# Kernel optimization log

Measured on AMD Instinct MI355X. Metric: run time of the kernel, lower is better.

Reference implementation:

```python
import jax, jax.numpy as jnp
import numpy as np

T = 4096          # tokens (batch*seq)
DIM = 2048        # model dim
INTER = 1024      # moe_inter_dim
E = 32            # n_routed_experts
TOPK = 6          # n_activated_experts
G = 8             # n_expert_groups
TOPK_G = 4        # n_limited_groups
SHARED_INTER = 2 * INTER  # n_shared_experts * moe_inter_dim
ROUTE_SCALE = 1.0


def setup_inputs() -> dict:
    key = jax.random.key(0)
    ks = jax.random.split(key, 8)
    s = 0.02
    return {
        "x": jax.random.normal(ks[0], (T, DIM), jnp.float32),
        "gate_w": jax.random.normal(ks[1], (E, DIM), jnp.float32) * s,
        "wg": jax.random.normal(ks[2], (E, DIM, INTER), jnp.float32) * s,   # gate_proj (stored [in,out])
        "wu": jax.random.normal(ks[3], (E, DIM, INTER), jnp.float32) * s,   # up_proj
        "wd": jax.random.normal(ks[4], (E, INTER, DIM), jnp.float32) * s,   # down_proj
        "swg": jax.random.normal(ks[5], (DIM, SHARED_INTER), jnp.float32) * s,
        "swu": jax.random.normal(ks[6], (DIM, SHARED_INTER), jnp.float32) * s,
        "swd": jax.random.normal(ks[7], (SHARED_INTER, DIM), jnp.float32) * s,
    }


def _gate(x, gate_w):
    # scores = softmax(x @ W^T); bias is None since dim != 7168 -> group score = amax
    scores = jax.nn.softmax(x @ gate_w.T, axis=-1)          # [T, E]
    orig = scores
    gs = scores.reshape(x.shape[0], G, E // G)              # [T, G, E/G]
    group_scores = gs.max(axis=-1)                          # [T, G]
    _, gidx = jax.lax.top_k(group_scores, TOPK_G)           # [T, TOPK_G]
    gmask = jnp.zeros((x.shape[0], G), bool).at[
        jnp.arange(x.shape[0])[:, None], gidx].set(True)
    masked = jnp.where(gmask[:, :, None], gs, -jnp.inf).reshape(x.shape[0], E)
    _, idx = jax.lax.top_k(masked, TOPK)                    # [T, TOPK]
    w = jnp.take_along_axis(orig, idx, axis=1) * ROUTE_SCALE  # softmax path: no renorm
    return w, idx


def reference(x, gate_w, wg, wu, wd, swg, swu, swd):
    weights, indices = _gate(x, gate_w)
    # combine[t, e] = routing weight of expert e for token t (0 if not selected)
    combine = (jax.nn.one_hot(indices, E, dtype=x.dtype) * weights[..., None]).sum(axis=1)  # [T, E]
    y = jnp.zeros_like(x)
    for e in range(E):  # fixed small loop over structurally distinct expert params
        h = jax.nn.silu(x @ wg[e]) * (x @ wu[e])            # [T, INTER]
        y = y + (h @ wd[e]) * combine[:, e:e + 1]
    shared = (jax.nn.silu(x @ swg) * (x @ swu)) @ swd       # shared experts MLP
    return y + shared
```

## Files before the change

kernel.cpp:

```cpp
#include <hip/hip_runtime.h>
#include <hip/hip_bf16.h>

typedef float f32x4 __attribute__((ext_vector_type(4)));
typedef __bf16 bf16x8 __attribute__((ext_vector_type(8)));
typedef unsigned short u16;

#define T_TOK 4096
#define DIMK 2048
#define INTERN 1024
#define NEXP 32
#define NTOPK 6
#define NGRP 8
#define NTOPG 4
#define SINTER 2048
#define MAXPADROWS 29184

__device__ __forceinline__ void glds16(const void* g, void* l) {
    auto* gp = (const __attribute__((address_space(1))) int*)(g);
    auto* lp = (__attribute__((address_space(3))) int*)(l);
    __builtin_amdgcn_global_load_lds(gp, lp, 16, 0, 0);
}

__device__ __forceinline__ size_t toff(int row, int k, int K) {
    int g = (k >> 3) & 7;
// ... 109 lines not shown
    float mx = sc[0];
#pragma unroll
    for (int e = 1; e < NEXP; ++e) mx = fmaxf(mx, sc[e]);
    float ssum = 0.f;
#pragma unroll
    for (int e = 0; e < NEXP; ++e) { sc[e] = __expf(sc[e] - mx); ssum += sc[e]; }
    const float inv = 1.f / ssum;
    float gsc[NGRP];
#pragma unroll
    for (int g = 0; g < NGRP; ++g) {
        float m2 = sc[g * 4];
#pragma unroll
        for (int j = 1; j < 4; ++j) m2 = fmaxf(m2, sc[g * 4 + j]);
        gsc[g] = m2;
    }
    int gsel = 0;
    for (int r = 0; r < NTOPG; ++r) {
        float bv = -1.f; int bi = 0;
#pragma unroll
        for (int g = 0; g < NGRP; ++g) {
            bool c = (((gsel >> g) & 1) == 0) && (gsc[g] > bv);
            bv = c ? gsc[g] : bv; bi = c ? g : bi;
        }
        gsel |= (1 << bi);
    }
    float msk[NEXP];
#pragma unroll
    for (int e = 0; e < NEXP; ++e) msk[e] = ((gsel >> (e >> 2)) & 1) ? sc[e] : -1.f;
    for (int r = 0; r < NTOPK; ++r) {
        float bv = -3.f; int bi = 0;
#pragma unroll
        for (int e = 0; e < NEXP; ++e) {
            bool c = msk[e] > bv;
            bv = c ? msk[e] : bv; bi = c ? e : bi;
        }
#pragma unroll
        for (int e = 0; e < NEXP; ++e) if (e == bi) msk[e] = -2.f;
        float w = bv * inv;
        int slot = atomicAdd(&counts[bi], 1);
        ids[bi * T_TOK + slot] = t;
        tok2row[t * NTOPK + r] = (bi << 12) | slot;
        wtok[t * NTOPK + r] = w;
    }
}

__global__ void scan_kernel(const int* __restrict__ counts, int* __restrict__ poff) {
    if (threadIdx.x == 0) {
        int o = 0;
        for (int e = 0; e < NEXP; ++e) { poff[e] = o; o += (counts[e] + 127) & ~127; }
    }
}


__global__ __launch_bounds__(1024, 1) void gemm1_fused_kernel(
    const u16* __restrict__ xbT, const u16* __restrict__ WcatE, u16* __restrict__ H,
    const u16* __restrict__ WcatS, u16* __restrict__ Hs,
    const int* __restrict__ counts, const int* __restrict__ poff, const int* __restrict__ ids) {
    __shared__ u16 Alds[2 * 16384];
    __shared__ u16 Blds[2 * 16384];
    constexpr int NT = DIMK / 64;

    int bm, bn, M, Mpad, hbase, HKdim, e = 0;
    const u16* b0;
    u16* ho;
    bool gath;
    if (blockIdx.z < 32) {
        int lin = blockIdx.x + 16 * (blockIdx.y + 8 * blockIdx.z);
        e = 31 - (((lin >> 10) << 3) | (lin & 7));
        int j = (lin >> 3) & 127;
        bm = j & 15; bn = j >> 4;
        M = counts[e];
        if (bm * 256 >= M) return;
        Mpad = (M + 127) & ~127;
        hbase = poff[e];
        b0 = WcatE + (size_t)e * 2048 * DIMK;
        ho = H; HKdim = INTERN; gath = true;
    } else {
        int lin = blockIdx.x + 16 * (blockIdx.y + 8 * (blockIdx.z - 32));
        int swz = (lin & 7) * 32 + (lin >> 3);
        bm = swz & 15; bn = swz >> 4;
        M = T_TOK; Mpad = T_TOK; hbase = 0;
        b0 = WcatS; ho = Hs; HKdim = SINTER; gath = false;
    }

    const int tid = threadIdx.x;
    const int srow = tid >> 3, sp = tid & 7;
    size_t aSrc[2];
#pragma unroll
    for (int h = 0; h < 2; ++h) {
        int row = bm * 256 + h * 128 + srow;
        int tok;
        if (gath) { int cr = row < M ? row : M - 1; tok = ids[e * T_TOK + cr]; }
        else tok = row;
        int gsw = sp ^ (srow & 7) ^ (tok & 7);
        aSrc[h] = (size_t)(tok >> 7) * (128 * 2048) + (size_t)((tok & 127) * 64 + (gsw << 3));
    }
    const u16* bCh[2] = { b0 + (size_t)(2 * bn + 0) * (128 * 2048), b0 + (size_t)(2 * bn + 1) * (128 * 2048) };
    const int t8 = tid * 8;

    const int lane = tid & 63, wv = tid >> 6;
    const int wr = wv >> 2, wc = wv & 3;
    const int l15 = lane & 15, lk = lane >> 4;

    f32x4 acc[4][4];
#pragma unroll
    for (int m = 0; m < 4; ++m)
#pragma unroll
        for (int n = 0; n < 4; ++n) acc[m][n] = {0.f, 0.f, 0.f, 0.f};

    auto STGALL = [&](int kt, int buf) {
        glds16(xbT + aSrc[0] + (size_t)kt * 8192, &Alds[buf * 16384 + t8]);
        glds16(xbT + aSrc[1] + (size_t)kt * 8192, &Alds[buf * 16384 + 8192 + t8]);
        glds16(bCh[0] + (size_t)kt * 8192 + t8, &Blds[buf * 16384 + t8]);
        glds16(bCh[1] + (size_t)kt * 8192 + t8, &Blds[buf * 16384 + 8192 + t8]);
    };
    bf16x8 afr[4][2], bfr[2][2];
    auto DSRA = [&](int buf) {
#pragma unroll
        for (int mi = 0; mi < 4; ++mi)
#pragma unroll
            for (int ki = 0; ki < 2; ++ki) {
                int rl = wr * 64 + mi * 16 + l15;
                int g = ki * 4 + lk;
                afr[mi][ki] = *reinterpret_cast<const bf16x8*>(
                    &Alds[buf * 16384 + (rl >> 7) * 8192 + (rl & 127) * 64 + ((g ^ (rl & 7)) << 3)]);
            }
    };
    auto DSRB = [&](int buf, int nh) {
#pragma unroll
        for (int nj = 0; nj < 2; ++nj)
#pragma unroll
            for (int ki = 0; ki < 2; ++ki) {
                int rc = wc * 64 + (nh * 2 + nj) * 16 + l15;
                int g = ki * 4 + lk;
                bfr[nj][ki] = *reinterpret_cast<const bf16x8*>(
                    &Blds[buf * 16384 + (rc >> 7) * 8192 + (rc & 127) * 64 + ((g ^ (rc & 7)) << 3)]);
            }
    };

    STGALL(0, 0);
    STGALL(1, 1);

#pragma unroll 1
    for (int i = 0; i < NT; ++i) {
        const int buf = i & 1;
        if (i + 1 < NT) {
            asm volatile("s_waitcnt vmcnt(4)" ::: "memory");
        } else {
            asm volatile("s_waitcnt vmcnt(0)" ::: "memory");
        }
        __builtin_amdgcn_s_barrier();
        __builtin_amdgcn_sched_barrier(0);
        DSRA(buf);
        DSRB(buf, 0);
        __builtin_amdgcn_s_setprio(1);
#pragma unroll
        for (int ki = 0; ki < 2; ++ki)
#pragma unroll
            for (int mi = 0; mi < 4; ++mi)
#pragma unroll
                for (int nj = 0; nj < 2; ++nj)
                    acc[mi][nj] = __builtin_amdgcn_mfma_f32_16x16x32_bf16(afr[mi][ki], bfr[nj][ki], acc[mi][nj], 0, 0, 0);
        __builtin_amdgcn_s_setprio(0);
        DSRB(buf, 1);
        __builtin_amdgcn_s_setprio(1);
#pragma unroll
        for (int ki = 0; ki < 2; ++ki)
#pragma unroll
            for (int mi = 0; mi < 4; ++mi)
#pragma unroll
                for (int nj = 0; nj < 2; ++nj)
                    acc[mi][2 + nj] = __builtin_amdgcn_mfma_f32_16x16x32_bf16(afr[mi][ki], bfr[nj][ki], acc[mi][2 + nj], 0, 0, 0);
        __builtin_amdgcn_s_setprio(0);
        __builtin_amdgcn_sched_barrier(0);
        __builtin_amdgcn_s_barrier();
        __builtin_amdgcn_sched_barrier(0);
        if (i + 2 < NT) STGALL(i + 2, buf);
    }

#pragma unroll
    for (int mi = 0; mi < 4; ++mi) {
#pragma unroll
        for (int r = 0; r < 4; ++r) {
            int grow = bm * 256 + wr * 64 + mi * 16 + lk * 4 + r;
            if (grow < Mpad) {
#pragma unroll
                for (int nh = 0; nh < 2; ++nh) {
                    float gg = acc[mi][nh * 2 + 0][r];
                    float uu = acc[mi][nh * 2 + 1][r];
                    float h = gg / (1.f + __expf(-gg)) * uu;
                    int n = bn * 256 + wc * 64 + nh * 32 + l15;
                    int jcol = ((n >> 5) << 4) + (n & 15);
                    __bf16 hb = (__bf16)h;
                    ho[toff(hbase + grow, jcol, HKdim)] = __builtin_bit_cast(u16, hb);
                }
            }
        }
    }
}

__global__ __launch_bounds__(1024, 1) void gemm2_fused_kernel(
    const u16* __restrict__ H, const u16* __restrict__ wdT, u16* __restrict__ Ye,
    const u16* __restrict__ Hs, const u16* __restrict__ swdT, u16* __restrict__ Yss,
    const int* __restrict__ counts, const int* __restrict__ poff) {
    __shared__ u16 Alds[2 * 16384];
    __shared__ u16 Blds[2 * 16384];
    constexpr int NT = 16;

    int bm, bn, M, rowbase, AKK, kt0;
    const u16 *aBase, *bBase;
    u16* yo;
    if (blockIdx.z < 32) {
        int lin = blockIdx.x + 16 * (blockIdx.y + 8 * blockIdx.z);
        int e = 31 - (((lin >> 10) << 3) | (lin & 7));
        int j = (lin >> 3) & 127;
        bm = j & 15; bn = j >> 4;
        M = counts[e];
        if (bm * 256 >= M) return;
        rowbase = poff[e];
        aBase = H + (size_t)poff[e] * INTERN;
        bBase = wdT + (size_t)e * 2048 * INTERN;
        yo = Ye; AKK = INTERN; kt0 = 0;
    } else {
        int lin = blockIdx.x + 16 * (blockIdx.y + 8 * (blockIdx.z - 32));
        int swz = (lin & 7) * 32 + (lin >> 3);
        bm = swz & 15; bn = (swz >> 4) & 7;
        int ks = swz >> 7;
        M = T_TOK; rowbase = ks * T_TOK;
        aBase = Hs; bBase = swdT; yo = Yss; AKK = SINTER; kt0 = ks * 16;
    }
    const u16* aCh[2] = { aBase + (size_t)(2 * bm + 0) * (size_t)(128 * AKK) + (size_t)kt0 * 8192,
                          aBase + (size_t)(2 * bm + 1) * (size_t)(128 * AKK) + (size_t)kt0 * 8192 };
    const u16* bCh[2] = { bBase + (size_t)(2 * bn + 0) * (size_t)(128 * AKK) + (size_t)kt0 * 8192,
                          bBase + (size_t)(2 * bn + 1) * (size_t)(128 * AKK) + (size_t)kt0 * 8192 };
    const int tid = threadIdx.x;
    const int t8 = tid * 8;
    const int lane = tid & 63, wv = tid >> 6;
    const int wr = wv >> 2, wc = wv & 3;
    const int l15 = lane & 15, lk = lane >> 4;

    f32x4 acc[4][4];
#pragma unroll
    for (int m = 0; m < 4; ++m)
#pragma unroll
        for (int n = 0; n < 4; ++n) acc[m][n] = {0.f, 0.f, 0.f, 0.f};

    auto STGALL = [&](int kt, int buf) {
        glds16(aCh[0] + (size_t)kt * 8192 + t8, &Alds[buf * 16384 + t8]);
        glds16(aCh[1] + (size_t)kt * 8192 + t8, &Alds[buf * 16384 + 8192 + t8]);
        glds16(bCh[0] + (size_t)kt * 8192 + t8, &Blds[buf * 16384 + t8]);
        glds16(bCh[1] + (size_t)kt * 8192 + t8, &Blds[buf * 16384 + 8192 + t8]);
    };
    bf16x8 afr[4][2], bfr[2][2];
    auto DSRA = [&](int buf) {
#pragma unroll
        for (int mi = 0; mi < 4; ++mi)
#pragma unroll
            for (int ki = 0; ki < 2; ++ki) {
                int rl = wr * 64 + mi * 16 + l15;
                int g = ki * 4 + lk;
                afr[mi][ki] = *reinterpret_cast<const bf16x8*>(
                    &Alds[buf * 16384 + (rl >> 7) * 8192 + (rl & 127) * 64 + ((g ^ (rl & 7)) << 3)]);
            }
    };
    auto DSRB = [&](int buf, int nh) {
#pragma unroll
        for (int nj = 0; nj < 2; ++nj)
#pragma unroll
            for (int ki = 0; ki < 2; ++ki) {
                int rc = wc * 64 + (nh * 2 + nj) * 16 + l15;
                int g = ki * 4 + lk;
                bfr[nj][ki] = *reinterpret_cast<const bf16x8*>(
                    &Blds[buf * 16384 + (rc >> 7) * 8192 + (rc & 127) * 64 + ((g ^ (rc & 7)) << 3)]);
            }
    };

    STGALL(0, 0);
    STGALL(1, 1);

#pragma unroll 1
    for (int i = 0; i < NT; ++i) {
        const int buf = i & 1;
        if (i + 1 < NT) {
            asm volatile("s_waitcnt vmcnt(4)" ::: "memory");
        } else {
            asm volatile("s_waitcnt vmcnt(0)" ::: "memory");
        }
        __builtin_amdgcn_s_barrier();
        __builtin_amdgcn_sched_barrier(0);
        DSRA(buf);
        DSRB(buf, 0);
        __builtin_amdgcn_s_setprio(1);
#pragma unroll
        for (int ki = 0; ki < 2; ++ki)
#pragma unroll
            for (int mi = 0; mi < 4; ++mi)
#pragma unroll
                for (int nj = 0; nj < 2; ++nj)
                    acc[mi][nj] = __builtin_amdgcn_mfma_f32_16x16x32_bf16(afr[mi][ki], bfr[nj][ki], acc[mi][nj], 0, 0, 0);
        __builtin_amdgcn_s_setprio(0);
        DSRB(buf, 1);
        __builtin_amdgcn_s_setprio(1);
#pragma unroll
        for (int ki = 0; ki < 2; ++ki)
#pragma unroll
            for (int mi = 0; mi < 4; ++mi)
#pragma unroll
                for (int nj = 0; nj < 2; ++nj)
                    acc[mi][2 + nj] = __builtin_amdgcn_mfma_f32_16x16x32_bf16(afr[mi][ki], bfr[nj][ki], acc[mi][2 + nj], 0, 0, 0);
        __builtin_amdgcn_s_setprio(0);
        __builtin_amdgcn_sched_barrier(0);
        __builtin_amdgcn_s_barrier();
        __builtin_amdgcn_sched_barrier(0);
        if (i + 2 < NT) STGALL(i + 2, buf);
    }

#pragma unroll
    for (int mi = 0; mi < 4; ++mi) {
#pragma unroll
        for (int r = 0; r < 4; ++r) {
            int grow = bm * 256 + wr * 64 + mi * 16 + lk * 4 + r;
            if (grow < M) {
                u16* yr = yo + (size_t)(rowbase + grow) * 2048;
#pragma unroll
                for (int ni = 0; ni < 4; ++ni) {
                    int col = bn * 256 + wc * 64 + ni * 16 + l15;
                    __bf16 yb = (__bf16)acc[mi][ni][r];
                    yr[col] = __builtin_bit_cast(u16, yb);
                }
            }
        }
    }
}

__global__ __launch_bounds__(256) void combine_kernel(const u16* __restrict__ Yss, const u16* __restrict__ Ye,
                                                      const int* __restrict__ tok2row, const float* __restrict__ wtok,
                                                      const int* __restrict__ poff, float* __restrict__ out) {
    const int t = blockIdx.x;
    const int c = threadIdx.x * 8;
    bf16x8 v0 = *reinterpret_cast<const bf16x8*>(Yss + (size_t)t * 2048 + c);
    bf16x8 v1 = *reinterpret_cast<const bf16x8*>(Yss + (size_t)(T_TOK + t) * 2048 + c);
    float acc[8];
#pragma unroll
    for (int j = 0; j < 8; ++j) acc[j] = (float)v0[j] + (float)v1[j];
#pragma unroll
    for (int r = 0; r < NTOPK; ++r) {
        int pk = tok2row[t * NTOPK + r];
        int e = pk >> 12, sl = pk & 4095;
        int row = poff[e] + sl;
        float w = wtok[t * NTOPK + r];
        bf16x8 v = *reinterpret_cast<const bf16x8*>(Ye + (size_t)row * 2048 + c);
#pragma unroll
        for (int j = 0; j < 8; ++j) acc[j] += w * (float)v[j];
    }
    float4 o0 = {acc[0], acc[1], acc[2], acc[3]};
    float4 o1 = {acc[4], acc[5], acc[6], acc[7]};
    float4* po = reinterpret_cast<float4*>(out + (size_t)t * 2048 + c);
    po[0] = o0; po[1] = o1;
}

extern "C" void kernel_launch(void* const* d_in, const int* in_sizes, int n_in,
                              void* d_out, int out_size, void* d_ws, size_t ws_size,
                              hipStream_t stream) {
    const float* x = (const float*)d_in[0];
    const float* gate_w = (const float*)d_in[1];
    const float* wg = (const float*)d_in[2];
    const float* wu = (const float*)d_in[3];
    const float* wd = (const float*)d_in[4];
    const float* swg = (const float*)d_in[5];
    const float* swu = (const float*)d_in[6];
    const float* swd = (const float*)d_in[7];
    float* out = (float*)d_out;

    char* ws = (char*)d_ws;
    size_t off = 0;
    auto alloc = [&](size_t bytes) {
        void* p = ws + off;
        off = (off + bytes + 255) & ~(size_t)255;
        return p;
    };
    u16* xbT = (u16*)alloc((size_t)T_TOK * DIMK * 2);
    u16* H = (u16*)alloc((size_t)MAXPADROWS * INTERN * 2);
    u16* Hs = (u16*)alloc((size_t)T_TOK * SINTER * 2);
    u16* Ye = (u16*)alloc((size_t)MAXPADROWS * 2048 * 2);
    u16* Yss = (u16*)alloc((size_t)2 * T_TOK * 2048 * 2);
    int* ids = (int*)alloc((size_t)NEXP * T_TOK * 4);
    int* tok2row = (int*)alloc((size_t)T_TOK * NTOPK * 4);
    float* wtok = (float*)alloc((size_t)T_TOK * NTOPK * 4);
    int* counts = (int*)alloc(NEXP * 4);
    int* poff = (int*)alloc(NEXP * 4);
    u16* WcatS = (u16*)alloc((size_t)(2 * SINTER) * DIMK * 2);
    u16* swdT = (u16*)alloc((size_t)DIMK * SINTER * 2);
    u16* WcatE = (u16*)alloc((size_t)NEXP * (2 * INTERN) * DIMK * 2);
    u16* wdT = WcatE;

    hipMemsetAsync(counts, 0, NEXP * 4, stream);
    cast_x_tiled_kernel<<<(T_TOK * DIMK) / (256 * 8), 256, 0, stream>>>(x, xbT);
    gate_kernel<<<T_TOK, 64, 0, stream>>>(x, gate_w, counts, ids, tok2row, wtok);
    scan_kernel<<<1, 64, 0, stream>>>(counts, poff);

    cat_trans_kernel<DIMK, SINTER><<<dim3(SINTER / 32, DIMK / 64, 1), 256, 0, stream>>>(swg, swu, WcatS);
    cat_trans_kernel<DIMK, INTERN><<<dim3(INTERN / 32, DIMK / 64, NEXP), 256, 0, stream>>>(wg, wu, WcatE);
    trans_tiled_kernel<SINTER, DIMK><<<dim3(DIMK / 64, SINTER / 64, 1), 256, 0, stream>>>(swd, swdT);

    gemm1_fused_kernel<<<dim3(16, 8, 34), 1024, 0, stream>>>(
        xbT, WcatE, H, WcatS, Hs, counts, poff, ids);

    trans_tiled_kernel<INTERN, DIMK><<<dim3(DIMK / 64, INTERN / 64, NEXP), 256, 0, stream>>>(wd, wdT);

    gemm2_fused_kernel<<<dim3(16, 8, 34), 1024, 0, stream>>>(
        H, wdT, Ye, Hs, swdT, Yss, counts, poff);

    combine_kernel<<<T_TOK, 256, 0, stream>>>(Yss, Ye, tok2row, wtok, poff, out);
}
```

Baseline: 1.137 ms.

## Use 8-wave blocks with 128x64 warp tiles and interleaved staged prefetch

Both grouped GEMMs go from 16 waves to 8 waves per block. Each wave now computes a 128x64 sub-tile with twice as many accumulators. The main loop is split into four MFMA phases, and the next k-tile's A and B halves are loaded between them, in a ping-pong style schedule that overlaps global-to-LDS copies with compute. Launch bounds now allow two blocks per CU to raise occupancy, at the cost of more registers per wave and extra barriers.

```diff
diff --git a/kernel.cpp b/kernel.cpp
--- a/kernel.cpp
+++ b/kernel.cpp
@@ -185,7 +185,7 @@
 }
 
 
-__global__ __launch_bounds__(1024, 1) void gemm1_fused_kernel(
+__global__ __launch_bounds__(512, 2) void gemm1_fused_kernel(
     const u16* __restrict__ xbT, const u16* __restrict__ WcatE, u16* __restrict__ H,
     const u16* __restrict__ WcatS, u16* __restrict__ Hs,
     const int* __restrict__ counts, const int* __restrict__ poff, const int* __restrict__ ids) {
@@ -217,110 +217,136 @@
     }
 
     const int tid = threadIdx.x;
-    const int srow = tid >> 3, sp = tid & 7;
-    size_t aSrc[2];
-#pragma unroll
-    for (int h = 0; h < 2; ++h) {
-        int row = bm * 256 + h * 128 + srow;
-        int tok;
-        if (gath) { int cr = row < M ? row : M - 1; tok = ids[e * T_TOK + cr]; }
-        else tok = row;
-        int gsw = sp ^ (srow & 7) ^ (tok & 7);
-        aSrc[h] = (size_t)(tok >> 7) * (128 * 2048) + (size_t)((tok & 127) * 64 + (gsw << 3));
-    }
+    const int t8 = tid * 8;
+    size_t aSrc[2][2];
+#pragma unroll
+    for (int h = 0; h < 2; ++h)
+#pragma unroll
+        for (int j = 0; j < 2; ++j) {
+            int drow = j * 64 + (tid >> 3);
+            int row = bm * 256 + h * 128 + drow;
+            int tok;
+            if (gath) { int cr = row < M ? row : M - 1; tok = ids[e * T_TOK + cr]; }
+            else tok = row;
+            int slot = (tid & 7) ^ (drow & 7) ^ (tok & 7);
+            aSrc[h][j] = (size_t)(tok >> 7) * (size_t)(128 * 2048) + (size_t)((tok & 127) * 64 + slot * 8);
+        }
     const u16* bCh[2] = { b0 + (size_t)(2 * bn + 0) * (128 * 2048), b0 + (size_t)(2 * bn + 1) * (128 * 2048) };
-    const int t8 = tid * 8;
 
     const int lane = tid & 63, wv = tid >> 6;
     const int wr = wv >> 2, wc = wv & 3;
     const int l15 = lane & 15, lk = lane >> 4;
 
-    f32x4 acc[4][4];
-#pragma unroll
-    for (int m = 0; m < 4; ++m)
+    f32x4 acc[8][4];
+#pragma unroll
+    for (int m = 0; m < 8; ++m)
 #pragma unroll
         for (int n = 0; n < 4; ++n) acc[m][n] = {0.f, 0.f, 0.f, 0.f};
 
-    auto STGALL = [&](int kt, int buf) {
-        glds16(xbT + aSrc[0] + (size_t)kt * 8192, &Alds[buf * 16384 + t8]);
-        glds16(xbT + aSrc[1] + (size_t)kt * 8192, &Alds[buf * 16384 + 8192 + t8]);
-        glds16(bCh[0] + (size_t)kt * 8192 + t8, &Blds[buf * 16384 + t8]);
-        glds16(bCh[1] + (size_t)kt * 8192 + t8, &Blds[buf * 16384 + 8192 + t8]);
-    };
-    bf16x8 afr[4][2], bfr[2][2];
-    auto DSRA = [&](int buf) {
+    auto SA = [&](int kt, int h, int buf) {
+        glds16(xbT + aSrc[h][0] + (size_t)kt * 8192, &Alds[buf * 16384 + h * 8192 + t8]);
+        glds16(xbT + aSrc[h][1] + (size_t)kt * 8192, &Alds[buf * 16384 + h * 8192 + 4096 + t8]);
+    };
+    auto SB = [&](int kt, int h, int buf) {
+        glds16(bCh[h] + (size_t)kt * 8192 + t8, &Blds[buf * 16384 + h * 8192 + t8]);
+        glds16(bCh[h] + (size_t)kt * 8192 + 4096 + t8, &Blds[buf * 16384 + h * 8192 + 4096 + t8]);
+    };
+    bf16x8 afr[4][2], bfr0[2][2], bfr1[2][2];
+    auto DSRA = [&](int buf, int mh) {
 #pragma unroll
         for (int mi = 0; mi < 4; ++mi)
 #pragma unroll
             for (int ki = 0; ki < 2; ++ki) {
-                int rl = wr * 64 + mi * 16 + l15;
+                int rl = wr * 128 + mh * 64 + mi * 16 + l15;
                 int g = ki * 4 + lk;
                 afr[mi][ki] = *reinterpret_cast<const bf16x8*>(
                     &Alds[buf * 16384 + (rl >> 7) * 8192 + (rl & 127) * 64 + ((g ^ (rl & 7)) << 3)]);
             }
     };
-    auto DSRB = [&](int buf, int nh) {
+    auto DSRB = [&](int buf, int nh, bf16x8 (&bf)[2][2]) {
 #pragma unroll
         for (int nj = 0; nj < 2; ++nj)
 #pragma unroll
             for (int ki = 0; ki < 2; ++ki) {
                 int rc = wc * 64 + (nh * 2 + nj) * 16 + l15;
                 int g = ki * 4 + lk;
-                bfr[nj][ki] = *reinterpret_cast<const bf16x8*>(
+                bf[nj][ki] = *reinterpret_cast<const bf16x8*>(
                     &Blds[buf * 16384 + (rc >> 7) * 8192 + (rc & 127) * 64 + ((g ^ (rc & 7)) << 3)]);
             }
     };
 
-    STGALL(0, 0);
-    STGALL(1, 1);
+    SA(0, 0, 0); SA(0, 1, 0); SB(0, 0, 0); SB(0, 1, 0); SA(1, 0, 1);
+    asm volatile("s_waitcnt vmcnt(2)" ::: "memory");
+    __builtin_amdgcn_s_barrier();
 
 #pragma unroll 1
-    for (int i = 0; i < NT; ++i) {
-        const int buf = i & 1;
-        if (i + 1 < NT) {
-            asm volatile("s_waitcnt vmcnt(4)" ::: "memory");
-        } else {
-            asm volatile("s_waitcnt vmcnt(0)" ::: "memory");
-        }
-        __builtin_amdgcn_s_barrier();
-        __builtin_amdgcn_sched_barrier(0);
-        DSRA(buf);
-        DSRB(buf, 0);
-        __builtin_amdgcn_s_setprio(1);
-#pragma unroll
-        for (int ki = 0; ki < 2; ++ki)
-#pragma unroll
-            for (int mi = 0; mi < 4; ++mi)
-#pragma unroll
-                for (int nj = 0; nj < 2; ++nj)
-                    acc[mi][nj] = __builtin_amdgcn_mfma_f32_16x16x32_bf16(afr[mi][ki], bfr[nj][ki], acc[mi][nj], 0, 0, 0);
-        __builtin_amdgcn_s_setprio(0);
-        DSRB(buf, 1);
-        __builtin_amdgcn_s_setprio(1);
-#pragma unroll
-        for (int ki = 0; ki < 2; ++ki)
-#pragma unroll
-            for (int mi = 0; mi < 4; ++mi)
-#pragma unroll
-                for (int nj = 0; nj < 2; ++nj)
-                    acc[mi][2 + nj] = __builtin_amdgcn_mfma_f32_16x16x32_bf16(afr[mi][ki], bfr[nj][ki], acc[mi][2 + nj], 0, 0, 0);
-        __builtin_amdgcn_s_setprio(0);
-        __builtin_amdgcn_sched_barrier(0);
-        __builtin_amdgcn_s_barrier();
-        __builtin_amdgcn_sched_barrier(0);
-        if (i + 2 < NT) STGALL(i + 2, buf);
-    }
-
-#pragma unroll
-    for (int mi = 0; mi < 4; ++mi) {
+    for (int t = 0; t < NT; ++t) {
+        const int buf = t & 1;
+        DSRA(buf, 0);
+        DSRB(buf, 0, bfr0);
+        if (t + 1 < NT) SA(t + 1, 1, buf ^ 1);
+        __builtin_amdgcn_s_barrier();
+        __builtin_amdgcn_s_setprio(1);
+#pragma unroll
+        for (int ki = 0; ki < 2; ++ki)
+#pragma unroll
+            for (int mi = 0; mi < 4; ++mi)
+#pragma unroll
+                for (int nj = 0; nj < 2; ++nj)
+                    acc[mi][nj] = __builtin_amdgcn_mfma_f32_16x16x32_bf16(afr[mi][ki], bfr0[nj][ki], acc[mi][nj], 0, 0, 0);
+        __builtin_amdgcn_s_setprio(0);
+        __builtin_amdgcn_s_barrier();
+        DSRB(buf, 1, bfr1);
+        if (t + 1 < NT) SB(t + 1, 0, buf ^ 1);
+        __builtin_amdgcn_s_barrier();
+        __builtin_amdgcn_s_setprio(1);
+#pragma unroll
+        for (int ki = 0; ki < 2; ++ki)
+#pragma unroll
+            for (int mi = 0; mi < 4; ++mi)
+#pragma unroll
+                for (int nj = 0; nj < 2; ++nj)
+                    acc[mi][2 + nj] = __builtin_amdgcn_mfma_f32_16x16x32_bf16(afr[mi][ki], bfr1[nj][ki], acc[mi][2 + nj], 0, 0, 0);
+        __builtin_amdgcn_s_setprio(0);
+        __builtin_amdgcn_s_barrier();
+        DSRA(buf, 1);
+        if (t + 1 < NT) SB(t + 1, 1, buf ^ 1);
+        __builtin_amdgcn_s_barrier();
+        __builtin_amdgcn_s_setprio(1);
+#pragma unroll
+        for (int ki = 0; ki < 2; ++ki)
+#pragma unroll
+            for (int mi = 0; mi < 4; ++mi)
+#pragma unroll
+                for (int nj = 0; nj < 2; ++nj)
+                    acc[4 + mi][2 + nj] = __builtin_amdgcn_mfma_f32_16x16x32_bf16(afr[mi][ki], bfr1[nj][ki], acc[4 + mi][2 + nj], 0, 0, 0);
+        __builtin_amdgcn_s_setprio(0);
+        __builtin_amdgcn_s_barrier();
+        if (t + 2 < NT) SA(t + 2, 0, buf);
+        __builtin_amdgcn_s_setprio(1);
+#pragma unroll
+        for (int ki = 0; ki < 2; ++ki)
+#pragma unroll
+            for (int mi = 0; mi < 4; ++mi)
+#pragma unroll
+                for (int nj = 0; nj < 2; ++nj)
+                    acc[4 + mi][nj] = __builtin_amdgcn_mfma_f32_16x16x32_bf16(afr[mi][ki], bfr0[nj][ki], acc[4 + mi][nj], 0, 0, 0);
+        __builtin_amdgcn_s_setprio(0);
+        if (t + 2 < NT) { asm volatile("s_waitcnt vmcnt(2)" ::: "memory"); }
+        else { asm volatile("s_waitcnt vmcnt(0)" ::: "memory"); }
+        __builtin_amdgcn_s_barrier();
+    }
+
+#pragma unroll
+    for (int mI = 0; mI < 8; ++mI) {
 #pragma unroll
         for (int r = 0; r < 4; ++r) {
-            int grow = bm * 256 + wr * 64 + mi * 16 + lk * 4 + r;
+            int grow = bm * 256 + wr * 128 + mI * 16 + lk * 4 + r;
             if (grow < Mpad) {
 #pragma unroll
                 for (int nh = 0; nh < 2; ++nh) {
-                    float gg = acc[mi][nh * 2 + 0][r];
-                    float uu = acc[mi][nh * 2 + 1][r];
+                    float gg = acc[mI][nh * 2 + 0][r];
+                    float uu = acc[mI][nh * 2 + 1][r];
                     float h = gg / (1.f + __expf(-gg)) * uu;
                     int n = bn * 256 + wc * 64 + nh * 32 + l15;
                     int jcol = ((n >> 5) << 4) + (n & 15);
@@ -332,7 +358,7 @@
     }
 }
 
-__global__ __launch_bounds__(1024, 1) void gemm2_fused_kernel(
+__global__ __launch_bounds__(512, 2) void gemm2_fused_kernel(
     const u16* __restrict__ H, const u16* __restrict__ wdT, u16* __restrict__ Ye,
     const u16* __restrict__ Hs, const u16* __restrict__ swdT, u16* __restrict__ Yss,
     const int* __restrict__ counts, const int* __restrict__ poff) {
@@ -372,93 +398,117 @@
     const int wr = wv >> 2, wc = wv & 3;
     const int l15 = lane & 15, lk = lane >> 4;
 
-    f32x4 acc[4][4];
-#pragma unroll
-    for (int m = 0; m < 4; ++m)
+    f32x4 acc[8][4];
+#pragma unroll
+    for (int m = 0; m < 8; ++m)
 #pragma unroll
         for (int n = 0; n < 4; ++n) acc[m][n] = {0.f, 0.f, 0.f, 0.f};
 
-    auto STGALL = [&](int kt, int buf) {
-        glds16(aCh[0] + (size_t)kt * 8192 + t8, &Alds[buf * 16384 + t8]);
-        glds16(aCh[1] + (size_t)kt * 8192 + t8, &Alds[buf * 16384 + 8192 + t8]);
-        glds16(bCh[0] + (size_t)kt * 8192 + t8, &Blds[buf * 16384 + t8]);
-        glds16(bCh[1] + (size_t)kt * 8192 + t8, &Blds[buf * 16384 + 8192 + t8]);
-    };
-    bf16x8 afr[4][2], bfr[2][2];
-    auto DSRA = [&](int buf) {
+    auto SA = [&](int kt, int h, int buf) {
+        glds16(aCh[h] + (size_t)kt * 8192 + t8, &Alds[buf * 16384 + h * 8192 + t8]);
+        glds16(aCh[h] + (size_t)kt * 8192 + 4096 + t8, &Alds[buf * 16384 + h * 8192 + 4096 + t8]);
+    };
+    auto SB = [&](int kt, int h, int buf) {
+        glds16(bCh[h] + (size_t)kt * 8192 + t8, &Blds[buf * 16384 + h * 8192 + t8]);
+        glds16(bCh[h] + (size_t)kt * 8192 + 4096 + t8, &Blds[buf * 16384 + h * 8192 + 4096 + t8]);
+    };
+    bf16x8 afr[4][2], bfr0[2][2], bfr1[2][2];
+    auto DSRA = [&](int buf, int mh) {
 #pragma unroll
         for (int mi = 0; mi < 4; ++mi)
 #pragma unroll
             for (int ki = 0; ki < 2; ++ki) {
-                int rl = wr * 64 + mi * 16 + l15;
+                int rl = wr * 128 + mh * 64 + mi * 16 + l15;
                 int g = ki * 4 + lk;
                 afr[mi][ki] = *reinterpret_cast<const bf16x8*>(
                     &Alds[buf * 16384 + (rl >> 7) * 8192 + (rl & 127) * 64 + ((g ^ (rl & 7)) << 3)]);
             }
     };
-    auto DSRB = [&](int buf, int nh) {
+    auto DSRB = [&](int buf, int nh, bf16x8 (&bf)[2][2]) {
 #pragma unroll
         for (int nj = 0; nj < 2; ++nj)
 #pragma unroll
             for (int ki = 0; ki < 2; ++ki) {
                 int rc = wc * 64 + (nh * 2 + nj) * 16 + l15;
                 int g = ki * 4 + lk;
-                bfr[nj][ki] = *reinterpret_cast<const bf16x8*>(
+                bf[nj][ki] = *reinterpret_cast<const bf16x8*>(
                     &Blds[buf * 16384 + (rc >> 7) * 8192 + (rc & 127) * 64 + ((g ^ (rc & 7)) << 3)]);
             }
     };
 
-    STGALL(0, 0);
-    STGALL(1, 1);
+    SA(0, 0, 0); SA(0, 1, 0); SB(0, 0, 0); SB(0, 1, 0); SA(1, 0, 1);
+    asm volatile("s_waitcnt vmcnt(2)" ::: "memory");
+    __builtin_amdgcn_s_barrier();
 
 #pragma unroll 1
-    for (int i = 0; i < NT; ++i) {
-        const int buf = i & 1;
-        if (i + 1 < NT) {
-            asm volatile("s_waitcnt vmcnt(4)" ::: "memory");
-        } else {
-            asm volatile("s_waitcnt vmcnt(0)" ::: "memory");
-        }
-        __builtin_amdgcn_s_barrier();
-        __builtin_amdgcn_sched_barrier(0);
-        DSRA(buf);
-        DSRB(buf, 0);
-        __builtin_amdgcn_s_setprio(1);
-#pragma unroll
-        for (int ki = 0; ki < 2; ++ki)
-#pragma unroll
-            for (int mi = 0; mi < 4; ++mi)
-#pragma unroll
-                for (int nj = 0; nj < 2; ++nj)
-                    acc[mi][nj] = __builtin_amdgcn_mfma_f32_16x16x32_bf16(afr[mi][ki], bfr[nj][ki], acc[mi][nj], 0, 0, 0);
-        __builtin_amdgcn_s_setprio(0);
-        DSRB(buf, 1);
-        __builtin_amdgcn_s_setprio(1);
-#pragma unroll
-        for (int ki = 0; ki < 2; ++ki)
-#pragma unroll
-            for (int mi = 0; mi < 4; ++mi)
-#pragma unroll
-                for (int nj = 0; nj < 2; ++nj)
-                    acc[mi][2 + nj] = __builtin_amdgcn_mfma_f32_16x16x32_bf16(afr[mi][ki], bfr[nj][ki], acc[mi][2 + nj], 0, 0, 0);
-        __builtin_amdgcn_s_setprio(0);
-        __builtin_amdgcn_sched_barrier(0);
-        __builtin_amdgcn_s_barrier();
-        __builtin_amdgcn_sched_barrier(0);
-        if (i + 2 < NT) STGALL(i + 2, buf);
-    }
-
-#pragma unroll
-    for (int mi = 0; mi < 4; ++mi) {
+    for (int t = 0; t < NT; ++t) {
+        const int buf = t & 1;
+        DSRA(buf, 0);
+        DSRB(buf, 0, bfr0);
+        if (t + 1 < NT) SA(t + 1, 1, buf ^ 1);
+        __builtin_amdgcn_s_barrier();
+        __builtin_amdgcn_s_setprio(1);
+#pragma unroll
+        for (int ki = 0; ki < 2; ++ki)
+#pragma unroll
+            for (int mi = 0; mi < 4; ++mi)
+#pragma unroll
+                for (int nj = 0; nj < 2; ++nj)
+                    acc[mi][nj] = __builtin_amdgcn_mfma_f32_16x16x32_bf16(afr[mi][ki], bfr0[nj][ki], acc[mi][nj], 0, 0, 0);
+        __builtin_amdgcn_s_setprio(0);
+        __builtin_amdgcn_s_barrier();
+        DSRB(buf, 1, bfr1);
+        if (t + 1 < NT) SB(t + 1, 0, buf ^ 1);
+        __builtin_amdgcn_s_barrier();
+        __builtin_amdgcn_s_setprio(1);
+#pragma unroll
+        for (int ki = 0; ki < 2; ++ki)
+#pragma unroll
+            for (int mi = 0; mi < 4; ++mi)
+#pragma unroll
+                for (int nj = 0; nj < 2; ++nj)
+                    acc[mi][2 + nj] = __builtin_amdgcn_mfma_f32_16x16x32_bf16(afr[mi][ki], bfr1[nj][ki], acc[mi][2 + nj], 0, 0, 0);
+        __builtin_amdgcn_s_setprio(0);
+        __builtin_amdgcn_s_barrier();
+        DSRA(buf, 1);
+        if (t + 1 < NT) SB(t + 1, 1, buf ^ 1);
+        __builtin_amdgcn_s_barrier();
+        __builtin_amdgcn_s_setprio(1);
+#pragma unroll
+        for (int ki = 0; ki < 2; ++ki)
+#pragma unroll
+            for (int mi = 0; mi < 4; ++mi)
+#pragma unroll
+                for (int nj = 0; nj < 2; ++nj)
+                    acc[4 + mi][2 + nj] = __builtin_amdgcn_mfma_f32_16x16x32_bf16(afr[mi][ki], bfr1[nj][ki], acc[4 + mi][2 + nj], 0, 0, 0);
+        __builtin_amdgcn_s_setprio(0);
+        __builtin_amdgcn_s_barrier();
+        if (t + 2 < NT) SA(t + 2, 0, buf);
+        __builtin_amdgcn_s_setprio(1);
+#pragma unroll
+        for (int ki = 0; ki < 2; ++ki)
+#pragma unroll
+            for (int mi = 0; mi < 4; ++mi)
+#pragma unroll
+                for (int nj = 0; nj < 2; ++nj)
+                    acc[4 + mi][nj] = __builtin_amdgcn_mfma_f32_16x16x32_bf16(afr[mi][ki], bfr0[nj][ki], acc[4 + mi][nj], 0, 0, 0);
+        __builtin_amdgcn_s_setprio(0);
+        if (t + 2 < NT) { asm volatile("s_waitcnt vmcnt(2)" ::: "memory"); }
+        else { asm volatile("s_waitcnt vmcnt(0)" ::: "memory"); }
+        __builtin_amdgcn_s_barrier();
+    }
+
+#pragma unroll
+    for (int mI = 0; mI < 8; ++mI) {
 #pragma unroll
         for (int r = 0; r < 4; ++r) {
-            int grow = bm * 256 + wr * 64 + mi * 16 + lk * 4 + r;
+            int grow = bm * 256 + wr * 128 + mI * 16 + lk * 4 + r;
             if (grow < M) {
                 u16* yr = yo + (size_t)(rowbase + grow) * 2048;
 #pragma unroll
                 for (int ni = 0; ni < 4; ++ni) {
                     int col = bn * 256 + wc * 64 + ni * 16 + l15;
-                    __bf16 yb = (__bf16)acc[mi][ni][r];
+                    __bf16 yb = (__bf16)acc[mI][ni][r];
                     yr[col] = __builtin_bit_cast(u16, yb);
                 }
             }
@@ -536,12 +586,12 @@
     cat_trans_kernel<DIMK, INTERN><<<dim3(INTERN / 32, DIMK / 64, NEXP), 256, 0, stream>>>(wg, wu, WcatE);
     trans_tiled_kernel<SINTER, DIMK><<<dim3(DIMK / 64, SINTER / 64, 1), 256, 0, stream>>>(swd, swdT);
 
-    gemm1_fused_kernel<<<dim3(16, 8, 34), 1024, 0, stream>>>(
+    gemm1_fused_kernel<<<dim3(16, 8, 34), 512, 0, stream>>>(
         xbT, WcatE, H, WcatS, Hs, counts, poff, ids);
 
     trans_tiled_kernel<INTERN, DIMK><<<dim3(DIMK / 64, INTERN / 64, NEXP), 256, 0, stream>>>(wd, wdT);
 
-    gemm2_fused_kernel<<<dim3(16, 8, 34), 1024, 0, stream>>>(
+    gemm2_fused_kernel<<<dim3(16, 8, 34), 512, 0, stream>>>(
         H, wdT, Ye, Hs, swdT, Yss, counts, poff);
 
     combine_kernel<<<T_TOK, 256, 0, stream>>>(Yss, Ye, tok2row, wtok, poff, out);
```

New measurement: 1.034 ms. -9.0%, faster.

## Restructure MoE GEMMs to 256x128 tiles, BK=32, 512 threads, triple-buffered B

Applied to the files above, without the earlier changes.

Both grouped GEMM kernels move from 1024-thread blocks with 256x256 tiles and BK=64 to 512-thread blocks with 256x128 tiles and BK=32. The A tile is double-buffered and the B tile triple-buffered, and the next loads are issued before the MFMAs instead of after the barrier. With smaller LDS usage and launch_bounds(512,4), several blocks can share a CU and the grid doubles. The cost is lower per-block operand reuse and twice as many k-iterations, each with its own barrier.

```diff
diff --git a/kernel.cpp b/kernel.cpp
--- a/kernel.cpp
+++ b/kernel.cpp
@@ -185,22 +185,22 @@
 }
 
 
-__global__ __launch_bounds__(1024, 1) void gemm1_fused_kernel(
+__global__ __launch_bounds__(512, 4) void gemm1_fused_kernel(
     const u16* __restrict__ xbT, const u16* __restrict__ WcatE, u16* __restrict__ H,
     const u16* __restrict__ WcatS, u16* __restrict__ Hs,
     const int* __restrict__ counts, const int* __restrict__ poff, const int* __restrict__ ids) {
-    __shared__ u16 Alds[2 * 16384];
-    __shared__ u16 Blds[2 * 16384];
-    constexpr int NT = DIMK / 64;
+    __shared__ u16 Alds[2 * 8192];
+    __shared__ u16 Blds[3 * 4096];
+    constexpr int NT = DIMK / 32;
 
     int bm, bn, M, Mpad, hbase, HKdim, e = 0;
     const u16* b0;
     u16* ho;
     bool gath;
     if (blockIdx.z < 32) {
-        int lin = blockIdx.x + 16 * (blockIdx.y + 8 * blockIdx.z);
-        e = 31 - (((lin >> 10) << 3) | (lin & 7));
-        int j = (lin >> 3) & 127;
+        int lin = blockIdx.x + 16 * (blockIdx.y + 16 * blockIdx.z);
+        e = 31 - (((lin >> 11) << 3) | (lin & 7));
+        int j = (lin >> 3) & 255;
         bm = j & 15; bn = j >> 4;
         M = counts[e];
         if (bm * 256 >= M) return;
@@ -209,256 +209,263 @@
         b0 = WcatE + (size_t)e * 2048 * DIMK;
         ho = H; HKdim = INTERN; gath = true;
     } else {
-        int lin = blockIdx.x + 16 * (blockIdx.y + 8 * (blockIdx.z - 32));
-        int swz = (lin & 7) * 32 + (lin >> 3);
+        int lin = blockIdx.x + 16 * (blockIdx.y + 16 * (blockIdx.z - 32));
+        int swz = (lin & 7) * 64 + (lin >> 3);
         bm = swz & 15; bn = swz >> 4;
         M = T_TOK; Mpad = T_TOK; hbase = 0;
         b0 = WcatS; ho = Hs; HKdim = SINTER; gath = false;
     }
 
     const int tid = threadIdx.x;
-    const int srow = tid >> 3, sp = tid & 7;
-    size_t aSrc[2];
-#pragma unroll
-    for (int h = 0; h < 2; ++h) {
-        int row = bm * 256 + h * 128 + srow;
+    const int sdr = tid >> 2, ss = tid & 3;
+    size_t srcA[2][2];
+#pragma unroll
+    for (int j = 0; j < 2; ++j) {
+        int drow = j * 128 + sdr;
+        int arow = bm * 256 + drow;
         int tok;
-        if (gath) { int cr = row < M ? row : M - 1; tok = ids[e * T_TOK + cr]; }
-        else tok = row;
-        int gsw = sp ^ (srow & 7) ^ (tok & 7);
-        aSrc[h] = (size_t)(tok >> 7) * (128 * 2048) + (size_t)((tok & 127) * 64 + (gsw << 3));
-    }
-    const u16* bCh[2] = { b0 + (size_t)(2 * bn + 0) * (128 * 2048), b0 + (size_t)(2 * bn + 1) * (128 * 2048) };
-    const int t8 = tid * 8;
+        if (gath) { int cr = arow < M ? arow : M - 1; tok = ids[e * T_TOK + cr]; }
+        else tok = arow;
+        int g = ss ^ ((drow >> 1) & 3);
+#pragma unroll
+        for (int p = 0; p < 2; ++p) {
+            int gg = p * 4 + g;
+            srcA[j][p] = (size_t)(tok >> 7) * (size_t)(128 * 2048) + (size_t)((tok & 127) * 64 + ((gg ^ (tok & 7)) << 3));
+        }
+    }
+    const u16* bCh = b0 + (size_t)bn * (128 * DIMK);
+    int srcB[2];
+    {
+        int g = ss ^ ((sdr >> 1) & 3);
+#pragma unroll
+        for (int p = 0; p < 2; ++p) {
+            int gg = p * 4 + g;
+            srcB[p] = sdr * 64 + ((gg ^ (sdr & 7)) << 3);
+        }
+    }
 
     const int lane = tid & 63, wv = tid >> 6;
     const int wr = wv >> 2, wc = wv & 3;
     const int l15 = lane & 15, lk = lane >> 4;
 
-    f32x4 acc[4][4];
-#pragma unroll
-    for (int m = 0; m < 4; ++m)
-#pragma unroll
-        for (int n = 0; n < 4; ++n) acc[m][n] = {0.f, 0.f, 0.f, 0.f};
-
-    auto STGALL = [&](int kt, int buf) {
-        glds16(xbT + aSrc[0] + (size_t)kt * 8192, &Alds[buf * 16384 + t8]);
-        glds16(xbT + aSrc[1] + (size_t)kt * 8192, &Alds[buf * 16384 + 8192 + t8]);
-        glds16(bCh[0] + (size_t)kt * 8192 + t8, &Blds[buf * 16384 + t8]);
-        glds16(bCh[1] + (size_t)kt * 8192 + t8, &Blds[buf * 16384 + 8192 + t8]);
-    };
-    bf16x8 afr[4][2], bfr[2][2];
-    auto DSRA = [&](int buf) {
+    f32x4 acc[8][2];
+#pragma unroll
+    for (int m = 0; m < 8; ++m)
+#pragma unroll
+        for (int n = 0; n < 2; ++n) acc[m][n] = {0.f, 0.f, 0.f, 0.f};
+
+    auto SA = [&](int kt, int buf) {
+        const size_t cko = (size_t)(kt >> 1) * 8192;
+        const int p = kt & 1;
+        glds16(xbT + cko + srcA[0][p], &Alds[buf * 8192 + tid * 8]);
+        glds16(xbT + cko + srcA[1][p], &Alds[buf * 8192 + 4096 + tid * 8]);
+    };
+    auto SB = [&](int kt, int buf) {
+        glds16(bCh + (size_t)(kt >> 1) * 8192 + srcB[kt & 1], &Blds[buf * 4096 + tid * 8]);
+    };
+    bf16x8 afr[4], bfr[2];
+    auto DSRA = [&](int buf, int mb) {
+#pragma unroll
+        for (int mi = 0; mi < 4; ++mi) {
+            int rl = wr * 128 + (mb * 4 + mi) * 16 + l15;
+            afr[mi] = *reinterpret_cast<const bf16x8*>(
+                &Alds[buf * 8192 + rl * 32 + ((lk ^ ((rl >> 1) & 3)) << 3)]);
+        }
+    };
+    auto DSRB = [&](int buf) {
+#pragma unroll
+        for (int nj = 0; nj < 2; ++nj) {
+            int rc = wc * 32 + nj * 16 + l15;
+            bfr[nj] = *reinterpret_cast<const bf16x8*>(
+                &Blds[buf * 4096 + rc * 32 + ((lk ^ ((rc >> 1) & 3)) << 3)]);
+        }
+    };
+
+    SA(0, 0); SB(0, 0); SB(1, 1);
+    asm volatile("s_waitcnt vmcnt(1)" ::: "memory");
+    __builtin_amdgcn_s_barrier();
+
+#pragma unroll 1
+    for (int t = 0; t < NT; ++t) {
+        const int abuf = t & 1;
+        const int bbuf = t % 3;
+        DSRA(abuf, 0);
+        DSRB(bbuf);
+        if (t + 1 < NT) SA(t + 1, abuf ^ 1);
+        if (t + 2 < NT) SB(t + 2, (t + 2) % 3);
+        __builtin_amdgcn_s_setprio(1);
 #pragma unroll
         for (int mi = 0; mi < 4; ++mi)
 #pragma unroll
-            for (int ki = 0; ki < 2; ++ki) {
-                int rl = wr * 64 + mi * 16 + l15;
-                int g = ki * 4 + lk;
-                afr[mi][ki] = *reinterpret_cast<const bf16x8*>(
-                    &Alds[buf * 16384 + (rl >> 7) * 8192 + (rl & 127) * 64 + ((g ^ (rl & 7)) << 3)]);
+            for (int nj = 0; nj < 2; ++nj)
+                acc[mi][nj] = __builtin_amdgcn_mfma_f32_16x16x32_bf16(afr[mi], bfr[nj], acc[mi][nj], 0, 0, 0);
+        __builtin_amdgcn_s_setprio(0);
+        DSRA(abuf, 1);
+        __builtin_amdgcn_s_setprio(1);
+#pragma unroll
+        for (int mi = 0; mi < 4; ++mi)
+#pragma unroll
+            for (int nj = 0; nj < 2; ++nj)
+                acc[4 + mi][nj] = __builtin_amdgcn_mfma_f32_16x16x32_bf16(afr[mi], bfr[nj], acc[4 + mi][nj], 0, 0, 0);
+        __builtin_amdgcn_s_setprio(0);
+        if (t + 2 < NT) { asm volatile("s_waitcnt vmcnt(1)" ::: "memory"); }
+        else { asm volatile("s_waitcnt vmcnt(0)" ::: "memory"); }
+        __builtin_amdgcn_s_barrier();
+    }
+
+#pragma unroll
+    for (int mI = 0; mI < 8; ++mI) {
+#pragma unroll
+        for (int r = 0; r < 4; ++r) {
+            int grow = bm * 256 + wr * 128 + mI * 16 + lk * 4 + r;
+            if (grow < Mpad) {
+                float gg = acc[mI][0][r];
+                float uu = acc[mI][1][r];
+                float h = gg / (1.f + __expf(-gg)) * uu;
+                int jcol = (bn * 4 + wc) * 16 + l15;
+                __bf16 hb = (__bf16)h;
+                ho[toff(hbase + grow, jcol, HKdim)] = __builtin_bit_cast(u16, hb);
             }
-    };
-    auto DSRB = [&](int buf, int nh) {
-#pragma unroll
-        for (int nj = 0; nj < 2; ++nj)
-#pragma unroll
-            for (int ki = 0; ki < 2; ++ki) {
-                int rc = wc * 64 + (nh * 2 + nj) * 16 + l15;
-                int g = ki * 4 + lk;
-                bfr[nj][ki] = *reinterpret_cast<const bf16x8*>(
-                    &Blds[buf * 16384 + (rc >> 7) * 8192 + (rc & 127) * 64 + ((g ^ (rc & 7)) << 3)]);
-            }
-    };
-
-    STGALL(0, 0);
-    STGALL(1, 1);
-
-#pragma unroll 1
-    for (int i = 0; i < NT; ++i) {
-        const int buf = i & 1;
-        if (i + 1 < NT) {
-            asm volatile("s_waitcnt vmcnt(4)" ::: "memory");
-        } else {
-            asm volatile("s_waitcnt vmcnt(0)" ::: "memory");
-        }
-        __builtin_amdgcn_s_barrier();
-        __builtin_amdgcn_sched_barrier(0);
-        DSRA(buf);
-        DSRB(buf, 0);
-        __builtin_amdgcn_s_setprio(1);
-#pragma unroll
-        for (int ki = 0; ki < 2; ++ki)
-#pragma unroll
-            for (int mi = 0; mi < 4; ++mi)
-#pragma unroll
-                for (int nj = 0; nj < 2; ++nj)
-                    acc[mi][nj] = __builtin_amdgcn_mfma_f32_16x16x32_bf16(afr[mi][ki], bfr[nj][ki], acc[mi][nj], 0, 0, 0);
-        __builtin_amdgcn_s_setprio(0);
-        DSRB(buf, 1);
-        __builtin_amdgcn_s_setprio(1);
-#pragma unroll
-        for (int ki = 0; ki < 2; ++ki)
-#pragma unroll
-            for (int mi = 0; mi < 4; ++mi)
-#pragma unroll
-                for (int nj = 0; nj < 2; ++nj)
-                    acc[mi][2 + nj] = __builtin_amdgcn_mfma_f32_16x16x32_bf16(afr[mi][ki], bfr[nj][ki], acc[mi][2 + nj], 0, 0, 0);
-        __builtin_amdgcn_s_setprio(0);
-        __builtin_amdgcn_sched_barrier(0);
-        __builtin_amdgcn_s_barrier();
-        __builtin_amdgcn_sched_barrier(0);
-        if (i + 2 < NT) STGALL(i + 2, buf);
-    }
-
-#pragma unroll
-    for (int mi = 0; mi < 4; ++mi) {
-#pragma unroll
-        for (int r = 0; r < 4; ++r) {
-            int grow = bm * 256 + wr * 64 + mi * 16 + lk * 4 + r;
-            if (grow < Mpad) {
-#pragma unroll
-                for (int nh = 0; nh < 2; ++nh) {
-                    float gg = acc[mi][nh * 2 + 0][r];
-                    float uu = acc[mi][nh * 2 + 1][r];
-                    float h = gg / (1.f + __expf(-gg)) * uu;
-                    int n = bn * 256 + wc * 64 + nh * 32 + l15;
-                    int jcol = ((n >> 5) << 4) + (n & 15);
-                    __bf16 hb = (__bf16)h;
-                    ho[toff(hbase + grow, jcol, HKdim)] = __builtin_bit_cast(u16, hb);
-                }
-            }
-        }
-    }
-}
-
-__global__ __launch_bounds__(1024, 1) void gemm2_fused_kernel(
+        }
+    }
+}
+
+__global__ __launch_bounds__(512, 4) void gemm2_fused_kernel(
     const u16* __restrict__ H, const u16* __restrict__ wdT, u16* __restrict__ Ye,
     const u16* __restrict__ Hs, const u16* __restrict__ swdT, u16* __restrict__ Yss,
     const int* __restrict__ counts, const int* __restrict__ poff) {
-    __shared__ u16 Alds[2 * 16384];
-    __shared__ u16 Blds[2 * 16384];
-    constexpr int NT = 16;
-
-    int bm, bn, M, rowbase, AKK, kt0;
+    __shared__ u16 Alds[2 * 8192];
+    __shared__ u16 Blds[3 * 4096];
+    constexpr int NT = 32;
+
+    int bm, bn, M, rowbase, AKK, ck0;
     const u16 *aBase, *bBase;
     u16* yo;
     if (blockIdx.z < 32) {
-        int lin = blockIdx.x + 16 * (blockIdx.y + 8 * blockIdx.z);
-        int e = 31 - (((lin >> 10) << 3) | (lin & 7));
-        int j = (lin >> 3) & 127;
+        int lin = blockIdx.x + 16 * (blockIdx.y + 16 * blockIdx.z);
+        int e = 31 - (((lin >> 11) << 3) | (lin & 7));
+        int j = (lin >> 3) & 255;
         bm = j & 15; bn = j >> 4;
         M = counts[e];
         if (bm * 256 >= M) return;
         rowbase = poff[e];
         aBase = H + (size_t)poff[e] * INTERN;
         bBase = wdT + (size_t)e * 2048 * INTERN;
-        yo = Ye; AKK = INTERN; kt0 = 0;
+        yo = Ye; AKK = INTERN; ck0 = 0;
     } else {
-        int lin = blockIdx.x + 16 * (blockIdx.y + 8 * (blockIdx.z - 32));
-        int swz = (lin & 7) * 32 + (lin >> 3);
-        bm = swz & 15; bn = (swz >> 4) & 7;
-        int ks = swz >> 7;
+        int lin = blockIdx.x + 16 * (blockIdx.y + 16 * (blockIdx.z - 32));
+        int swz = (lin & 7) * 64 + (lin >> 3);
+        bm = swz & 15; bn = (swz >> 4) & 15;
+        int ks = swz >> 8;
         M = T_TOK; rowbase = ks * T_TOK;
-        aBase = Hs; bBase = swdT; yo = Yss; AKK = SINTER; kt0 = ks * 16;
-    }
-    const u16* aCh[2] = { aBase + (size_t)(2 * bm + 0) * (size_t)(128 * AKK) + (size_t)kt0 * 8192,
-                          aBase + (size_t)(2 * bm + 1) * (size_t)(128 * AKK) + (size_t)kt0 * 8192 };
-    const u16* bCh[2] = { bBase + (size_t)(2 * bn + 0) * (size_t)(128 * AKK) + (size_t)kt0 * 8192,
-                          bBase + (size_t)(2 * bn + 1) * (size_t)(128 * AKK) + (size_t)kt0 * 8192 };
+        aBase = Hs; bBase = swdT; yo = Yss; AKK = SINTER; ck0 = ks * 16;
+    }
     const int tid = threadIdx.x;
-    const int t8 = tid * 8;
+    const int sdr = tid >> 2, ss = tid & 3;
+    size_t srcA[2][2];
+#pragma unroll
+    for (int j = 0; j < 2; ++j) {
+        int lrow = bm * 256 + j * 128 + sdr;
+        int cr = (rowbase == 0 || true) ? lrow : lrow;
+        int g = ss ^ (((j * 128 + sdr) >> 1) & 3);
+#pragma unroll
+        for (int p = 0; p < 2; ++p) {
+            int gg = p * 4 + g;
+            srcA[j][p] = (size_t)(cr >> 7) * (size_t)(128 * AKK) + (size_t)((cr & 127) * 64 + ((gg ^ (cr & 7)) << 3));
+        }
+    }
+    const u16* bCh = bBase + (size_t)bn * (128 * AKK);
+    int srcB[2];
+    {
+        int g = ss ^ ((sdr >> 1) & 3);
+#pragma unroll
+        for (int p = 0; p < 2; ++p) {
+            int gg = p * 4 + g;
+            srcB[p] = sdr * 64 + ((gg ^ (sdr & 7)) << 3);
+        }
+    }
+    const size_t ckBase = (size_t)ck0 * 8192;
+
     const int lane = tid & 63, wv = tid >> 6;
     const int wr = wv >> 2, wc = wv & 3;
     const int l15 = lane & 15, lk = lane >> 4;
 
-    f32x4 acc[4][4];
-#pragma unroll
-    for (int m = 0; m < 4; ++m)
-#pragma unroll
-        for (int n = 0; n < 4; ++n) acc[m][n] = {0.f, 0.f, 0.f, 0.f};
-
-    auto STGALL = [&](int kt, int buf) {
-        glds16(aCh[0] + (size_t)kt * 8192 + t8, &Alds[buf * 16384 + t8]);
-        glds16(aCh[1] + (size_t)kt * 8192 + t8, &Alds[buf * 16384 + 8192 + t8]);
-        glds16(bCh[0] + (size_t)kt * 8192 + t8, &Blds[buf * 16384 + t8]);
-        glds16(bCh[1] + (size_t)kt * 8192 + t8, &Blds[buf * 16384 + 8192 + t8]);
-    };
-    bf16x8 afr[4][2], bfr[2][2];
-    auto DSRA = [&](int buf) {
+    f32x4 acc[8][2];
+#pragma unroll
+    for (int m = 0; m < 8; ++m)
+#pragma unroll
+        for (int n = 0; n < 2; ++n) acc[m][n] = {0.f, 0.f, 0.f, 0.f};
+
+    auto SA = [&](int kt, int buf) {
+        const size_t cko = ckBase + (size_t)(kt >> 1) * 8192;
+        const int p = kt & 1;
+        glds16(aBase + cko + srcA[0][p], &Alds[buf * 8192 + tid * 8]);
+        glds16(aBase + cko + srcA[1][p], &Alds[buf * 8192 + 4096 + tid * 8]);
+    };
+    auto SB = [&](int kt, int buf) {
+        glds16(bCh + ckBase + (size_t)(kt >> 1) * 8192 + srcB[kt & 1], &Blds[buf * 4096 + tid * 8]);
+    };
+    bf16x8 afr[4], bfr[2];
+    auto DSRA = [&](int buf, int mb) {
+#pragma unroll
+        for (int mi = 0; mi < 4; ++mi) {
+            int rl = wr * 128 + (mb * 4 + mi) * 16 + l15;
+            afr[mi] = *reinterpret_cast<const bf16x8*>(
+                &Alds[buf * 8192 + rl * 32 + ((lk ^ ((rl >> 1) & 3)) << 3)]);
+        }
+    };
+    auto DSRB = [&](int buf) {
+#pragma unroll
+        for (int nj = 0; nj < 2; ++nj) {
+            int rc = wc * 32 + nj * 16 + l15;
+            bfr[nj] = *reinterpret_cast<const bf16x8*>(
+                &Blds[buf * 4096 + rc * 32 + ((lk ^ ((rc >> 1) & 3)) << 3)]);
+        }
+    };
+
+    SA(0, 0); SB(0, 0); SB(1, 1);
+    asm volatile("s_waitcnt vmcnt(1)" ::: "memory");
+    __builtin_amdgcn_s_barrier();
+
+#pragma unroll 1
+    for (int t = 0; t < NT; ++t) {
+        const int abuf = t & 1;
+        const int bbuf = t % 3;
+        DSRA(abuf, 0);
+        DSRB(bbuf);
+        if (t + 1 < NT) SA(t + 1, abuf ^ 1);
+        if (t + 2 < NT) SB(t + 2, (t + 2) % 3);
+        __builtin_amdgcn_s_setprio(1);
 #pragma unroll
         for (int mi = 0; mi < 4; ++mi)
 #pragma unroll
-            for (int ki = 0; ki < 2; ++ki) {
-                int rl = wr * 64 + mi * 16 + l15;
-                int g = ki * 4 + lk;
-                afr[mi][ki] = *reinterpret_cast<const bf16x8*>(
-                    &Alds[buf * 16384 + (rl >> 7) * 8192 + (rl & 127) * 64 + ((g ^ (rl & 7)) << 3)]);
-            }
-    };
-    auto DSRB = [&](int buf, int nh) {
-#pragma unroll
-        for (int nj = 0; nj < 2; ++nj)
-#pragma unroll
-            for (int ki = 0; ki < 2; ++ki) {
-                int rc = wc * 64 + (nh * 2 + nj) * 16 + l15;
-                int g = ki * 4 + lk;
-                bfr[nj][ki] = *reinterpret_cast<const bf16x8*>(
-                    &Blds[buf * 16384 + (rc >> 7) * 8192 + (rc & 127) * 64 + ((g ^ (rc & 7)) << 3)]);
-            }
-    };
-
-    STGALL(0, 0);
-    STGALL(1, 1);
-
-#pragma unroll 1
-    for (int i = 0; i < NT; ++i) {
-        const int buf = i & 1;
-        if (i + 1 < NT) {
-            asm volatile("s_waitcnt vmcnt(4)" ::: "memory");
-        } else {
-            asm volatile("s_waitcnt vmcnt(0)" ::: "memory");
-        }
+            for (int nj = 0; nj < 2; ++nj)
+                acc[mi][nj] = __builtin_amdgcn_mfma_f32_16x16x32_bf16(afr[mi], bfr[nj], acc[mi][nj], 0, 0, 0);
+        __builtin_amdgcn_s_setprio(0);
+        DSRA(abuf, 1);
+        __builtin_amdgcn_s_setprio(1);
+#pragma unroll
+        for (int mi = 0; mi < 4; ++mi)
+#pragma unroll
+            for (int nj = 0; nj < 2; ++nj)
+                acc[4 + mi][nj] = __builtin_amdgcn_mfma_f32_16x16x32_bf16(afr[mi], bfr[nj], acc[4 + mi][nj], 0, 0, 0);
+        __builtin_amdgcn_s_setprio(0);
+        if (t + 2 < NT) { asm volatile("s_waitcnt vmcnt(1)" ::: "memory"); }
+        else { asm volatile("s_waitcnt vmcnt(0)" ::: "memory"); }
         __builtin_amdgcn_s_barrier();
-        __builtin_amdgcn_sched_barrier(0);
-        DSRA(buf);
-        DSRB(buf, 0);
-        __builtin_amdgcn_s_setprio(1);
-#pragma unroll
-        for (int ki = 0; ki < 2; ++ki)
-#pragma unroll
-            for (int mi = 0; mi < 4; ++mi)
-#pragma unroll
-                for (int nj = 0; nj < 2; ++nj)
-                    acc[mi][nj] = __builtin_amdgcn_mfma_f32_16x16x32_bf16(afr[mi][ki], bfr[nj][ki], acc[mi][nj], 0, 0, 0);
-        __builtin_amdgcn_s_setprio(0);
-        DSRB(buf, 1);
-        __builtin_amdgcn_s_setprio(1);
-#pragma unroll
-        for (int ki = 0; ki < 2; ++ki)
-#pragma unroll
-            for (int mi = 0; mi < 4; ++mi)
-#pragma unroll
-                for (int nj = 0; nj < 2; ++nj)
-                    acc[mi][2 + nj] = __builtin_amdgcn_mfma_f32_16x16x32_bf16(afr[mi][ki], bfr[nj][ki], acc[mi][2 + nj], 0, 0, 0);
-        __builtin_amdgcn_s_setprio(0);
-        __builtin_amdgcn_sched_barrier(0);
-        __builtin_amdgcn_s_barrier();
-        __builtin_amdgcn_sched_barrier(0);
-        if (i + 2 < NT) STGALL(i + 2, buf);
-    }
-
-#pragma unroll
-    for (int mi = 0; mi < 4; ++mi) {
+    }
+
+#pragma unroll
+    for (int mI = 0; mI < 8; ++mI) {
 #pragma unroll
         for (int r = 0; r < 4; ++r) {
-            int grow = bm * 256 + wr * 64 + mi * 16 + lk * 4 + r;
+            int grow = bm * 256 + wr * 128 + mI * 16 + lk * 4 + r;
             if (grow < M) {
                 u16* yr = yo + (size_t)(rowbase + grow) * 2048;
 #pragma unroll
-                for (int ni = 0; ni < 4; ++ni) {
-                    int col = bn * 256 + wc * 64 + ni * 16 + l15;
-                    __bf16 yb = (__bf16)acc[mi][ni][r];
+                for (int nj = 0; nj < 2; ++nj) {
+                    int col = bn * 128 + wc * 32 + nj * 16 + l15;
+                    __bf16 yb = (__bf16)acc[mI][nj][r];
                     yr[col] = __builtin_bit_cast(u16, yb);
                 }
             }
@@ -536,12 +543,12 @@
     cat_trans_kernel<DIMK, INTERN><<<dim3(INTERN / 32, DIMK / 64, NEXP), 256, 0, stream>>>(wg, wu, WcatE);
     trans_tiled_kernel<SINTER, DIMK><<<dim3(DIMK / 64, SINTER / 64, 1), 256, 0, stream>>>(swd, swdT);
 
-    gemm1_fused_kernel<<<dim3(16, 8, 34), 1024, 0, stream>>>(
+    gemm1_fused_kernel<<<dim3(16, 16, 34), 512, 0, stream>>>(
         xbT, WcatE, H, WcatS, Hs, counts, poff, ids);
 
     trans_tiled_kernel<INTERN, DIMK><<<dim3(DIMK / 64, INTERN / 64, NEXP), 256, 0, stream>>>(wd, wdT);
 
-    gemm2_fused_kernel<<<dim3(16, 8, 34), 1024, 0, stream>>>(
+    gemm2_fused_kernel<<<dim3(16, 16, 34), 512, 0, stream>>>(
         H, wdT, Ye, Hs, swdT, Yss, counts, poff);
 
     combine_kernel<<<T_TOK, 256, 0, stream>>>(Yss, Ye, tok2row, wtok, poff, out);
```

New measurement: 1.109 ms. 1.03x faster.
